# Optimization experiments

Measured on AMD Instinct MI355X. Metric: run time of the kernel, lower is better.

Reference implementation:

```python
import jax, jax.numpy as jnp
import numpy as np

N_NEAR = 16
BN_EPS = 1e-5


def fps(xyz, n_center):
    # farthest point sampling, deterministic start at index 0. xyz: [B,N,C]
    B, N, _ = xyz.shape
    dist0 = jnp.full((B, N), jnp.inf, dtype=xyz.dtype)
    far0 = jnp.zeros((B,), dtype=jnp.int32)

    def step(carry, _):
        dist, far = carry
        centroid = jnp.take_along_axis(xyz, far[:, None, None], axis=1)  # [B,1,C]
        d = jnp.sum((xyz - centroid) ** 2, axis=-1)                       # [B,N]
        dist = jnp.minimum(dist, d)
        nxt = jnp.argmax(dist, axis=-1).astype(jnp.int32)
        return (dist, nxt), far

    _, idxs = jax.lax.scan(step, (dist0, far0), None, length=n_center)
    return jnp.transpose(idxs)  # [B, n_center]


def knn(xyz, k):
    # k nearest neighbors (self included), xyz: [B,N,C] -> idx [B,N,k]
    sq = jnp.sum(xyz * xyz, axis=-1)
    d = sq[:, :, None] - 2.0 * jnp.einsum('bnc,bmc->bnm', xyz, xyz) + sq[:, None, :]
    _, idx = jax.lax.top_k(-d, k)
    return idx


def gather_points(x, idx):
    # x: [B,N,...], idx: [B,*dims] int -> [B,*dims,...]
    return jax.vmap(lambda xb, ib: xb[ib])(x, idx)


def conv_bn_relu(x, W, b, g, be):
    # x: [B,C,K,S]; 1x1 Conv2d + BatchNorm2d (training/batch stats) + ReLU
    y = jnp.einsum('oc,bcks->boks', W, x) + b[None, :, None, None]
    mean = jnp.mean(y, axis=(0, 2, 3), keepdims=True)
    var = jnp.mean((y - mean) ** 2, axis=(0, 2, 3), keepdims=True)  # biased var, as torch BN
    y = (y - mean) * jax.lax.rsqrt(var + BN_EPS)
    y = y * g[None, :, None, None] + be[None, :, None, None]
    return jax.nn.relu(y)


def setup_inputs() -> dict:
    key = jax.random.key(0)
    ks = jax.random.split(key, 8)
    B, N, EMB = 16, 2048, 64
    mlp = [64, 128, 256]
    in_ch = 2 + EMB
    inp = {
        'xy': jax.random.normal(ks[0], (B, 2, N), dtype=jnp.float32),
        'fea': jax.random.normal(ks[1], (B, EMB, N), dtype=jnp.float32),
    }
    last = in_ch
    for i, out in enumerate(mlp):
        inp[f'W{i+1}'] = 0.1 * jax.random.normal(ks[2 + i], (out, last), dtype=jnp.float32)
        inp[f'b{i+1}'] = jnp.zeros((out,), dtype=jnp.float32)
        inp[f'g{i+1}'] = jnp.ones((out,), dtype=jnp.float32)
        inp[f'be{i+1}'] = jnp.zeros((out,), dtype=jnp.float32)
        last = out
    return inp


def reference(xy, fea, W1, b1, g1, be1, W2, b2, g2, be2, W3, b3, g3, be3):
    B, _, N = xy.shape
    n_center = N // 2 + 1
    xyz = jnp.transpose(xy, (0, 2, 1))   # [B,N,2]
    f = jnp.transpose(fea, (0, 2, 1))    # [B,N,emb]

    fps_idx = fps(xyz, n_center)                      # [B,S]
    new_xyz = gather_points(xyz, fps_idx)             # [B,S,2]
    knn_idx = knn(xyz, N_NEAR)                        # [B,N,k]
    knn_of_fps = gather_points(knn_idx, fps_idx)      # [B,S,k]
    grouped_xyz = gather_points(xyz, knn_of_fps)      # [B,S,k,2]
    grouped_norm = grouped_xyz - new_xyz[:, :, None, :]
    grouped_f = gather_points(f, knn_of_fps)          # [B,S,k,emb]
    new_fea = jnp.concatenate([grouped_norm, grouped_f], axis=-1)  # [B,S,k,C]

    x = jnp.transpose(new_fea, (0, 3, 2, 1))          # [B,C,k,S]
    for (W, b, g, be) in ((W1, b1, g1, be1), (W2, b2, g2, be2), (W3, b3, g3, be3)):
        x = conv_bn_relu(x, W, b, g, be)
    out = jnp.max(x, axis=2)                          # [B,C_out,S]
    return jnp.transpose(new_xyz, (0, 2, 1)), out
```

## Files before the change

### kernel.cpp

```cpp
#include <hip/hip_runtime.h>
#include <math.h>

#define B_   16
#define N_   2048
#define S_   1025
#define K_   16
#define EMB_ 64
#define NF_  (B_ * S_ * K_)
#define NCH_ (NF_ / 64)
#define NBS_ (NCH_ * 4)

typedef float v2f __attribute__((ext_vector_type(2)));
typedef short bf16x8 __attribute__((ext_vector_type(8)));
typedef float f32x4 __attribute__((ext_vector_type(4)));

__device__ __forceinline__ unsigned short f2bf(float f) {
  unsigned u = __float_as_uint(f);
  u += 0x7fffu + ((u >> 16) & 1u);
  return (unsigned short)(u >> 16);
}
__device__ __forceinline__ float bfl(unsigned pk) { return __uint_as_float((pk & 0xffffu) << 16); }
__device__ __forceinline__ float bfh(unsigned pk) { return __uint_as_float(pk & 0xffff0000u); }

__global__ __launch_bounds__(256) __attribute__((amdgpu_waves_per_eu(1, 1)))
void fps_pk_kernel(const float* __restrict__ xy, const float* __restrict__ fea,
                   const float* __restrict__ W1,
                   const float* __restrict__ W2, const float* __restrict__ W3,
                   int* __restrict__ fps_idx, float* __restrict__ new_xyz,
                   float* __restrict__ out0, unsigned* __restrict__ Pp,
                   unsigned short* __restrict__ W2b, unsigned short* __restrict__ W3b) {
  __shared__ float smem[8192];
  if (blockIdx.x < 16) {
    const int b = blockIdx.x;
    float2* lxy = reinterpret_cast<float2*>(smem);
    const int lane = threadIdx.x;
    const float* xb = xy + (size_t)b * 2 * N_;
    v2f pxp[16], pyp[16];
    float dist[32];
    if (lane < 64) {
      const float2* xb2 = (const float2*)xb;
      const float2* yb2 = (const float2*)(xb + N_);
#pragma unroll
      for (int q = 0; q < 16; ++q) {
        float2 x01 = xb2[lane * 16 + q];
        float2 y01 = yb2[lane * 16 + q];
        int p = lane * 32 + 2 * q;
        lxy[p] = make_float2(x01.x, y01.x);
        lxy[p + 1] = make_float2(x01.y, y01.y);
        pxp[q][0] = x01.x; pxp[q][1] = x01.y;
        pyp[q][0] = y01.x; pyp[q][1] = y01.y;
        dist[2 * q] = __builtin_inff();
        dist[2 * q + 1] = __builtin_inff();
      }
#pragma unroll
      for (int q = 0; q < 16; ++q) {
        asm volatile("" : "+v"(pxp[q]), "+v"(pyp[q]));
      }
    }
    __syncthreads();
    if (lane < 64) {
      int cur = 0;
      for (int t = 0; t < S_; ++t) {
        float2 c = lxy[cur];
        if (lane == 0) {
          fps_idx[b * S_ + t] = cur;
          new_xyz[(b * S_ + t) * 2 + 0] = c.x;
          new_xyz[(b * S_ + t) * 2 + 1] = c.y;
          out0[b * 2 * S_ + t] = c.x;
          out0[b * 2 * S_ + S_ + t] = c.y;
        }
        const float ncx = -c.x, ncy = -c.y;
        v2f ncx2; ncx2[0] = ncx; ncx2[1] = ncx;
        v2f ncy2; ncy2[0] = ncy; ncy2[1] = ncy;
#pragma unroll
        for (int q = 0; q < 16; ++q) {
          v2f dx, dy, sx, sy, dd;
          asm("v_pk_add_f32 %0, %1, %2" : "=v"(dx) : "v"(pxp[q]), "v"(ncx2));
          asm("v_pk_add_f32 %0, %1, %2" : "=v"(dy) : "v"(pyp[q]), "v"(ncy2));
          asm("v_pk_mul_f32 %0, %1, %1" : "=v"(sx) : "v"(dx));
          asm("v_pk_mul_f32 %0, %1, %1" : "=v"(sy) : "v"(dy));
          asm("v_pk_add_f32 %0, %1, %2" : "=v"(dd) : "v"(sx), "v"(sy));
          dist[2 * q] = fminf(dist[2 * q], dd[0]);
          dist[2 * q + 1] = fminf(dist[2 * q + 1], dd[1]);
        }
        float m1[16], m2[8], m3[4], m4[2];
#pragma unroll
        for (int j = 0; j < 16; ++j) m1[j] = fmaxf(dist[2 * j], dist[2 * j + 1]);
#pragma unroll
        for (int j = 0; j < 8; ++j) m2[j] = fmaxf(m1[2 * j], m1[2 * j + 1]);
#pragma unroll
        for (int j = 0; j < 4; ++j) m3[j] = fmaxf(m2[2 * j], m2[2 * j + 1]);
        m4[0] = fmaxf(m3[0], m3[1]);
        m4[1] = fmaxf(m3[2], m3[3]);
        const float lmax = fmaxf(m4[0], m4[1]);
        int xr = __float_as_int(lmax);
#define DPP_MAX_STEP(CTRL)                                                        \
        {                                                                         \
          int tmp_ = __builtin_amdgcn_update_dpp(xr, xr, (CTRL), 0xF, 0xF, false);\
          xr = __float_as_int(fmaxf(__int_as_float(xr), __int_as_float(tmp_)));   \
        }
        DPP_MAX_STEP(0x111)
        DPP_MAX_STEP(0x112)
        DPP_MAX_STEP(0x114)
        DPP_MAX_STEP(0x118)
        DPP_MAX_STEP(0x142)
        DPP_MAX_STEP(0x143)
#undef DPP_MAX_STEP
        const float g = __int_as_float(__builtin_amdgcn_readlane(xr, 63));
        int n = (m4[0] == g) ? 0 : 1;
        float c3 = (n & 1) ? m3[2] : m3[0];
        n = 2 * n + ((c3 == g) ? 0 : 1);
        float lo2 = (n & 1) ? m2[2] : m2[0];
        float hi2 = (n & 1) ? m2[6] : m2[4];
        float c2 = (n & 2) ? hi2 : lo2;
        n = 2 * n + ((c2 == g) ? 0 : 1);
        float a0 = (n & 1) ? m1[2] : m1[0];
        float a1 = (n & 1) ? m1[6] : m1[4];
        float a2 = (n & 1) ? m1[10] : m1[8];
        float a3 = (n & 1) ? m1[14] : m1[12];
        float b0 = (n & 2) ? a1 : a0;
        float b1 = (n & 2) ? a3 : a2;
        float c1 = (n & 4) ? b1 : b0;
        n = 2 * n + ((c1 == g) ? 0 : 1);
        float e0 = (n & 1) ? dist[2] : dist[0];
        float e1 = (n & 1) ? dist[6] : dist[4];
        float e2 = (n & 1) ? dist[10] : dist[8];
        float e3 = (n & 1) ? dist[14] : dist[12];
        float e4 = (n & 1) ? dist[18] : dist[16];
        float e5 = (n & 1) ? dist[22] : dist[20];
        float e6 = (n & 1) ? dist[26] : dist[24];
        float e7 = (n & 1) ? dist[30] : dist[28];
        float f0 = (n & 2) ? e1 : e0;
        float f1 = (n & 2) ? e3 : e2;
        float f2 = (n & 2) ? e5 : e4;
        float f3 = (n & 2) ? e7 : e6;
        float g0 = (n & 4) ? f1 : f0;
        float g1 = (n & 4) ? f3 : f2;
        float c0 = (n & 8) ? g1 : g0;
        const int lf = 2 * n + ((c0 == g) ? 0 : 1);
        unsigned long long mask = __ballot(lmax == g);
        int first = __ffsll(mask) - 1;
        cur = __builtin_amdgcn_readlane(lane * 32 + lf, first);
      }
    }
  } else if (blockIdx.x < 528) {
    const int bid = blockIdx.x - 16;
    const int t = threadIdx.x;
    const int b = bid >> 5;
    const int pt0 = (bid & 31) << 6;
    float* W1L = smem;
    float* feaL = smem + 4096;
#pragma unroll
    for (int p = 0; p < 16; ++p) {
      int idx = t + 256 * p;
      int c = idx >> 6, e = idx & 63;
      W1L[e * 64 + c] = W1[c * 66 + 2 + e];
      int r = (t >> 6) + 4 * p, cc = t & 63;
      feaL[r * 64 + cc] = fea[((size_t)b * 64 + r) * N_ + pt0 + cc];
    }
    __syncthreads();
    const int tpt = t & 15, tcq = t >> 4;
    float acc[4][4];
#pragma unroll
    for (int i = 0; i < 4; ++i)
#pragma unroll
      for (int j = 0; j < 4; ++j) acc[i][j] = 0.f;
    for (int e = 0; e < 64; ++e) {
      float4 a4 = *reinterpret_cast<const float4*>(&W1L[e * 64 + tcq * 4]);
      float4 b4 = *reinterpret_cast<const float4*>(&feaL[e * 64 + tpt * 4]);
      const float av[4] = {a4.x, a4.y, a4.z, a4.w};
      const float bvv[4] = {b4.x, b4.y, b4.z, b4.w};
#pragma unroll
      for (int i = 0; i < 4; ++i)
#pragma unroll
        for (int j = 0; j < 4; ++j) acc[i][j] = fmaf(av[i], bvv[j], acc[i][j]);
    }
#pragma unroll
    for (int j = 0; j < 4; ++j) {
      int pt = tpt * 4 + j;
      unsigned lo = (unsigned)f2bf(acc[0][j]) | ((unsigned)f2bf(acc[1][j]) << 16);
      unsigned hi = (unsigned)f2bf(acc[2][j]) | ((unsigned)f2bf(acc[3][j]) << 16);
      unsigned* dst = &Pp[((size_t)(b * N_ + pt0 + pt)) * 32 + tcq * 2];
      dst[0] = lo;
      dst[1] = hi;
    }
  } else {
    const int t = threadIdx.x;
    for (int i = t; i < 128 * 64; i += 256) W2b[i] = f2bf(W2[i]);
    for (int i = t; i < 256 * 128; i += 256) W3b[i] = f2bf(W3[i]);
  }
}

__global__ __launch_bounds__(256) void knn_kernel(const float* __restrict__ xy,
                                                  const int* __restrict__ fps_idx,
                                                  int* __restrict__ knn_sel) {
  const int b = blockIdx.y;
  __shared__ float2 lxy[N_];
  __shared__ double lsq[N_];
  const float* xb = xy + (size_t)b * 2 * N_;
  for (int p = threadIdx.x; p < N_; p += 256) {
    float x = xb[p], y = xb[N_ + p];
    lxy[p] = make_float2(x, y);
    lsq[p] = (double)x * (double)x + (double)y * (double)y;
  }
  __syncthreads();
  const int t = threadIdx.x;
  const int s = blockIdx.x * 8 + (t >> 5);
  if (s >= S_) return;
  const int oct = t & 31;
  const int p0 = fps_idx[b * S_ + s];
  float2 q = lxy[p0];
  const double xn = (double)q.x, yn = (double)q.y;
  const double sqn = lsq[p0];
  double d16[16];
  int i16[16];
#pragma unroll
  for (int j = 0; j < 16; ++j) { d16[j] = __builtin_inf(); i16[j] = 0x7fffffff; }
  const int mlo = oct * 64;
  for (int m0 = mlo; m0 < mlo + 64; m0 += 4) {
    double dd[4];
#pragma unroll
    for (int u = 0; u < 4; ++u) {
      float2 p = lxy[m0 + u];
      double dot = (double)p.x * xn + (double)p.y * yn;
      dd[u] = (sqn - 2.0 * dot) + lsq[m0 + u];
    }
#pragma unroll
    for (int u = 0; u < 4; ++u) {
      if (dd[u] < d16[15]) {
        double d = dd[u];
        int mi = m0 + u;
#pragma unroll
        for (int j = 15; j >= 1; --j) {
          bool shift = d < d16[j - 1];
          bool ins = d < d16[j];
          d16[j] = shift ? d16[j - 1] : (ins ? d : d16[j]);
          i16[j] = shift ? i16[j - 1] : (ins ? mi : i16[j]);
        }
        if (d < d16[0]) { d16[0] = d; i16[0] = mi; }
      }
    }
  }
#pragma unroll
  for (int w = 1; w <= 16; w <<= 1) {
    double nd[16]; int ni[16];
#pragma unroll
    for (int i = 0; i < 16; ++i) {
      double rd = __shfl_xor(d16[15 - i], w, 64);
      int ri = __shfl_xor(i16[15 - i], w, 64);
      bool takeR = (rd < d16[i]) || (rd == d16[i] && ri < i16[i]);
      nd[i] = takeR ? rd : d16[i];
      ni[i] = takeR ? ri : i16[i];
    }
#pragma unroll
    for (int i = 0; i < 16; ++i) { d16[i] = nd[i]; i16[i] = ni[i]; }
    if (w < 16) {
#pragma unroll
      for (int dstg = 8; dstg >= 1; dstg >>= 1) {
#pragma unroll
        for (int i = 0; i < 16; ++i) {
          if ((i & dstg) == 0) {
            int a = i, c = i + dstg;
            bool sw = (d16[a] > d16[c]) || (d16[a] == d16[c] && i16[a] > i16[c]);
            double tlo = sw ? d16[c] : d16[a];
            double thi = sw ? d16[a] : d16[c];
            int ulo = sw ? i16[c] : i16[a];
            int uhi = sw ? i16[a] : i16[c];
            d16[a] = tlo; d16[c] = thi; i16[a] = ulo; i16[c] = uhi;
          }
        }
      }
    }
  }
  if (oct == 0) {
    int* dst = knn_sel + ((size_t)b * S_ + s) * K_;
#pragma unroll
    for (int j = 0; j < 16; ++j) dst[j] = i16[j];
  }
}

__global__ __launch_bounds__(256) void yk1_kernel(const float* __restrict__ xy,
                                                  const int* __restrict__ knn_sel,
                                                  const float* __restrict__ new_xyz,
                                                  const unsigned* __restrict__ Pp,
                                                  const float* __restrict__ W1,
                                                  const float* __restrict__ b1,
                                                  unsigned* __restrict__ Y1p) {
  __shared__ float w0s[64], w1s[64], bbs[64];
  const int t = threadIdx.x;
  if (t < 64) { w0s[t] = W1[t * 66 + 0]; w1s[t] = W1[t * 66 + 1]; bbs[t] = b1[t]; }
  __syncthreads();
  const int n = blockIdx.x * 256 + t;
  const int bs = n >> 4;
  const int b = bs / S_;
  const int nbr = knn_sel[n];
  const float dx = xy[(size_t)b * 2 * N_ + nbr] - new_xyz[bs * 2 + 0];
  const float dy = xy[(size_t)b * 2 * N_ + N_ + nbr] - new_xyz[bs * 2 + 1];
  const unsigned* prow = &Pp[((size_t)(b * N_ + nbr)) * 32];
#pragma unroll 8
  for (int j = 0; j < 32; ++j) {
    unsigned pj = prow[j];
    int c = 2 * j;
    float v0 = bfl(pj) + w0s[c] * dx + w1s[c] * dy + bbs[c];
    float v1 = bfh(pj) + w0s[c + 1] * dx + w1s[c + 1] * dy + bbs[c + 1];
    Y1p[(size_t)j * NF_ + n] = (unsigned)f2bf(v0) | ((unsigned)f2bf(v1) << 16);
  }
}

__global__ __launch_bounds__(256) void rowstats_kernel(const unsigned* __restrict__ Y1p,
                                                       float* __restrict__ parts) {
  const int j = blockIdx.x & 31;
  const int seg = blockIdx.x >> 5;
  const int SEG = NF_ / 8;
  const unsigned* p = Y1p + (size_t)j * NF_ + (size_t)seg * SEG;
  double s0 = 0, q0 = 0, s1 = 0, q1 = 0;
  for (int i = threadIdx.x; i < SEG; i += 256) {
    unsigned pk = p[i];
    double a = (double)bfl(pk), b = (double)bfh(pk);
    s0 += a; q0 = fma(a, a, q0);
    s1 += b; q1 = fma(b, b, q1);
  }
  __shared__ double sh[4][256];
  sh[0][threadIdx.x] = s0; sh[1][threadIdx.x] = q0;
  sh[2][threadIdx.x] = s1; sh[3][threadIdx.x] = q1;
  __syncthreads();
  for (int o = 128; o > 0; o >>= 1) {
    if (threadIdx.x < o) {
#pragma unroll
      for (int u = 0; u < 4; ++u) sh[u][threadIdx.x] += sh[u][threadIdx.x + o];
    }
    __syncthreads();
  }
  if (threadIdx.x == 0) {
    float* dst = parts + (size_t)(j * 8 + seg) * 4;
    dst[0] = (float)sh[0][0];
    dst[1] = (float)sh[2][0];
    dst[2] = (float)sh[1][0];
    dst[3] = (float)sh[3][0];
  }
}

__global__ void redabsch1_kernel(const float* __restrict__ parts,
                                 const float* __restrict__ g, const float* __restrict__ be,
                                 float* __restrict__ A, float* __restrict__ D) {
  int m = threadIdx.x;
  if (m >= 64) return;
  int j = m >> 1, par = m & 1;
  double a = 0.0, b = 0.0;
  for (int seg = 0; seg < 8; ++seg) {
    const float* src = parts + (size_t)(j * 8 + seg) * 4;
    a += (double)src[par];
    b += (double)src[2 + par];
  }
  double mu = a * (1.0 / NF_);
  double var = b * (1.0 / NF_) - mu * mu;
  double aa = (double)g[m] / sqrt(var + 1e-5);
  A[m] = (float)aa;
  D[m] = (float)((double)be[m] - aa * mu);
}

__global__ void redabsch_kernel(const float* __restrict__ parts, int P, int M,
                                const float* __restrict__ g, const float* __restrict__ be,
                                float* __restrict__ A, float* __restrict__ D) {
  int m = threadIdx.x;
  if (m >= M) return;
  double a = 0.0, b = 0.0;
  for (int p = 0; p < P; ++p) {
    a += (double)parts[(size_t)p * 2 * M + m];
    b += (double)parts[(size_t)p * 2 * M + M + m];
  }
  double mu = a * (1.0 / NF_);
  double var = b * (1.0 / NF_) - mu * mu;
  double aa = (double)g[m] / sqrt(var + 1e-5);
  A[m] = (float)aa;
  D[m] = (float)((double)be[m] - aa * mu);
}

__device__ __forceinline__ float rowsum16(float v) {
#define RADD(CTRL) { int tm_ = __builtin_amdgcn_update_dpp(0, __float_as_int(v), (CTRL), 0xF, 0xF, true); \
                     v += __int_as_float(tm_); }
  RADD(0x111) RADD(0x112) RADD(0x114) RADD(0x118)
#undef RADD
  return v;
}

__device__ __forceinline__ void stage_x1(const unsigned* Y1p, const float* ab1, char* x1c,
                                         size_t n0, int w, int L) {
#pragma unroll
  for (int e = 0; e < 8; ++e) {
    int k0 = 2 * (w + 4 * e);
    unsigned pkv = Y1p[(size_t)(k0 >> 1) * NF_ + n0 + L];
    float v0 = fmaxf(fmaf(bfl(pkv), ab1[k0], ab1[64 + k0]), 0.f);
    float v1 = fmaxf(fmaf(bfh(pkv), ab1[k0 + 1], ab1[64 + k0 + 1]), 0.f);
    unsigned pk = (unsigned)f2bf(v0) | ((unsigned)f2bf(v1) << 16);
    *reinterpret_cast<unsigned*>(&x1c[L * 128 + ((2 * k0) ^ ((L & 7) << 4))]) = pk;
  }
}

__global__ __launch_bounds__(256) void passA_mfma_kernel(
    const unsigned* __restrict__ Y1p, const unsigned short* __restrict__ W2b,
    const float* __restrict__ A1v, const float* __restrict__ Bc1v,
    float* __restrict__ parts) {
  __shared__ float ab1[128];
  __shared__ __align__(16) unsigned short x1b[64 * 64];
  const int t = threadIdx.x;
  const int w = t >> 6, L = t & 63;
  if (t < 128) ab1[t] = (t < 64) ? A1v[t] : Bc1v[t - 64];
  bf16x8 w2f[2][2];
#pragma unroll
  for (int rb = 0; rb < 2; ++rb)
#pragma unroll
    for (int ks = 0; ks < 2; ++ks) {
      int row = (2 * w + rb) * 16 + (L & 15);
      int koff = ks * 32 + (L >> 4) * 8;
      w2f[rb][ks] = *reinterpret_cast<const bf16x8*>(&W2b[row * 64 + koff]);
    }
  float vs[2][4], vq[2][4];
#pragma unroll
  for (int rb = 0; rb < 2; ++rb)
#pragma unroll
    for (int r = 0; r < 4; ++r) { vs[rb][r] = 0.f; vq[rb][r] = 0.f; }
  char* x1c = reinterpret_cast<char*>(x1b);
  for (int ch = blockIdx.x; ch < NCH_; ch += 512) {
    const size_t n0 = (size_t)ch * 64;
    __syncthreads();
    stage_x1(Y1p, ab1, x1c, n0, w, L);
    __syncthreads();
#pragma unroll
    for (int rb = 0; rb < 2; ++rb) {
      f32x4 acc2[4];
#pragma unroll
      for (int cb = 0; cb < 4; ++cb) acc2[cb][0] = acc2[cb][1] = acc2[cb][2] = acc2[cb][3] = 0.f;
#pragma unroll
      for (int ks = 0; ks < 2; ++ks)
#pragma unroll
        for (int cb = 0; cb < 4; ++cb) {
          int n = cb * 16 + (L & 15);
          int koff = ks * 32 + (L >> 4) * 8;
          bf16x8 bfr = *reinterpret_cast<const bf16x8*>(&x1c[n * 128 + ((2 * koff) ^ ((n & 7) << 4))]);
          acc2[cb] = __builtin_amdgcn_mfma_f32_16x16x32_bf16(w2f[rb][ks], bfr, acc2[cb], 0, 0, 0);
        }
#pragma unroll
      for (int cb = 0; cb < 4; ++cb)
#pragma unroll
        for (int r = 0; r < 4; ++r) {
          float y = acc2[cb][r];
          vs[rb][r] += y;
          vq[rb][r] = fmaf(y, y, vq[rb][r]);
        }
    }
  }
#pragma unroll
  for (int rb = 0; rb < 2; ++rb)
#pragma unroll
    for (int r = 0; r < 4; ++r) {
      float s = rowsum16(vs[rb][r]);
      float q = rowsum16(vq[rb][r]);
      if ((L & 15) == 15) {
        int row = (2 * w + rb) * 16 + (L >> 4) * 4 + r;
        parts[(size_t)blockIdx.x * 256 + row] = s;
        parts[(size_t)blockIdx.x * 256 + 128 + row] = q;
      }
    }
}

__global__ __launch_bounds__(256) void passB_mfma_kernel(
    const unsigned* __restrict__ Y1p,
    const unsigned short* __restrict__ W2b, const unsigned short* __restrict__ W3b,
    const float* __restrict__ A1v, const float* __restrict__ Bc1v,
    const float* __restrict__ A2v, const float* __restrict__ D2v,
    float* __restrict__ parts, unsigned* __restrict__ M3) {
  __shared__ float ab1[128];
  __shared__ __align__(16) unsigned short x1b[64 * 64];
  __shared__ __align__(16) unsigned short x2b[64 * 128];
  const int t = threadIdx.x;
  const int w = t >> 6, L = t & 63;
  if (t < 128) ab1[t] = (t < 64) ? A1v[t] : Bc1v[t - 64];
  bf16x8 w3f[4][4];
#pragma unroll
  for (int rb = 0; rb < 4; ++rb)
#pragma unroll
    for (int ks = 0; ks < 4; ++ks) {
      int row = (4 * w + rb) * 16 + (L & 15);
      int koff = ks * 32 + (L >> 4) * 8;
      w3f[rb][ks] = *reinterpret_cast<const bf16x8*>(&W3b[row * 128 + koff]);
    }
  bf16x8 w2f[2][2];
#pragma unroll
  for (int rb = 0; rb < 2; ++rb)
#pragma unroll
    for (int ks = 0; ks < 2; ++ks) {
      int row = (2 * w + rb) * 16 + (L & 15);
      int koff = ks * 32 + (L >> 4) * 8;
      w2f[rb][ks] = *reinterpret_cast<const bf16x8*>(&W2b[row * 64 + koff]);
    }
  float vs[4][4], vq[4][4];
#pragma unroll
  for (int rb = 0; rb < 4; ++rb)
#pragma unroll
    for (int r = 0; r < 4; ++r) { vs[rb][r] = 0.f; vq[rb][r] = 0.f; }
  char* x1c = reinterpret_cast<char*>(x1b);
  char* x2c = reinterpret_cast<char*>(x2b);
  for (int ch = blockIdx.x; ch < NCH_; ch += 256) {
    const size_t n0 = (size_t)ch * 64;
    __syncthreads();
    stage_x1(Y1p, ab1, x1c, n0, w, L);
    __syncthreads();
#pragma unroll
    for (int rb = 0; rb < 2; ++rb) {
      f32x4 acc2[4];
#pragma unroll
      for (int cb = 0; cb < 4; ++cb) acc2[cb][0] = acc2[cb][1] = acc2[cb][2] = acc2[cb][3] = 0.f;
#pragma unroll
      for (int ks = 0; ks < 2; ++ks)
#pragma unroll
        for (int cb = 0; cb < 4; ++cb) {
          int n = cb * 16 + (L & 15);
          int koff = ks * 32 + (L >> 4) * 8;
          bf16x8 bfr = *reinterpret_cast<const bf16x8*>(&x1c[n * 128 + ((2 * koff) ^ ((n & 7) << 4))]);
          acc2[cb] = __builtin_amdgcn_mfma_f32_16x16x32_bf16(w2f[rb][ks], bfr, acc2[cb], 0, 0, 0);
        }
#pragma unroll
      for (int cb = 0; cb < 4; ++cb) {
        int n = cb * 16 + (L & 15);
        int kbase = (2 * w + rb) * 16 + (L >> 4) * 4;
#pragma unroll
        for (int rp = 0; rp < 2; ++rp) {
          int r0 = 2 * rp;
          float a0 = A2v[kbase + r0], d0 = D2v[kbase + r0];
          float a1 = A2v[kbase + r0 + 1], d1 = D2v[kbase + r0 + 1];
          float v0 = fmaxf(fmaf(acc2[cb][r0], a0, d0), 0.f);
          float v1 = fmaxf(fmaf(acc2[cb][r0 + 1], a1, d1), 0.f);
          unsigned pk = (unsigned)f2bf(v0) | ((unsigned)f2bf(v1) << 16);
          int k0 = kbase + r0;
          *reinterpret_cast<unsigned*>(&x2c[n * 256 + ((2 * k0) ^ ((n & 7) << 4))]) = pk;
        }
      }
    }
    __syncthreads();
    bf16x8 b3[4][4];
#pragma unroll
    for (int cb = 0; cb < 4; ++cb)
#pragma unroll
      for (int ks = 0; ks < 4; ++ks) {
        int n = cb * 16 + (L & 15);
        int koff = ks * 32 + (L >> 4) * 8;
        b3[cb][ks] = *reinterpret_cast<const bf16x8*>(&x2c[n * 256 + ((2 * koff) ^ ((n & 7) << 4))]);
      }
#pragma unroll
    for (int rb = 0; rb < 4; ++rb) {
      f32x4 acc3[4];
#pragma unroll
      for (int cb = 0; cb < 4; ++cb) acc3[cb][0] = acc3[cb][1] = acc3[cb][2] = acc3[cb][3] = 0.f;
#pragma unroll
      for (int ks = 0; ks < 4; ++ks)
#pragma unroll
        for (int cb = 0; cb < 4; ++cb)
          acc3[cb] = __builtin_amdgcn_mfma_f32_16x16x32_bf16(w3f[rb][ks], b3[cb][ks], acc3[cb], 0, 0, 0);
#pragma unroll
      for (int cb = 0; cb < 4; ++cb)
#pragma unroll
        for (int r = 0; r < 4; ++r) {
          float y = acc3[cb][r];
          vs[rb][r] += y;
          vq[rb][r] = fmaf(y, y, vq[rb][r]);
        }
      {
        int rowbase = (4 * w + rb) * 16 + (L >> 4) * 4;
#pragma unroll
        for (int cb = 0; cb < 4; ++cb) {
#pragma unroll
          for (int r = 0; r < 4; ++r) {
            float v = acc3[cb][r];
            int xi = __float_as_int(v), xm = __float_as_int(v);
#define RMAX(CTRL) { int tm_ = __builtin_amdgcn_update_dpp(xi, xi, (CTRL), 0xF, 0xF, false); \
                     xi = __float_as_int(fmaxf(__int_as_float(xi), __int_as_float(tm_))); }
#define RMIN(CTRL) { int tm_ = __builtin_amdgcn_update_dpp(xm, xm, (CTRL), 0xF, 0xF, false); \
                     xm = __float_as_int(fminf(__int_as_float(xm), __int_as_float(tm_))); }
            RMAX(0x111) RMAX(0x112) RMAX(0x114) RMAX(0x118)
            RMIN(0x111) RMIN(0x112) RMIN(0x114) RMIN(0x118)
#undef RMAX
#undef RMIN
            if ((L & 15) == 15) {
              int row = rowbase + r;
              int bs = ch * 4 + cb;
              M3[(size_t)row * NBS_ + bs] =
                  (unsigned)f2bf(__int_as_float(xi)) | ((unsigned)f2bf(__int_as_float(xm)) << 16);
            }
          }
        }
      }
    }
  }
#pragma unroll
  for (int rb = 0; rb < 4; ++rb)
#pragma unroll
    for (int r = 0; r < 4; ++r) {
      float s = rowsum16(vs[rb][r]);
      float q = rowsum16(vq[rb][r]);
      if ((L & 15) == 15) {
        int row = (4 * w + rb) * 16 + (L >> 4) * 4 + r;
        parts[(size_t)blockIdx.x * 512 + row] = s;
        parts[(size_t)blockIdx.x * 512 + 256 + row] = q;
      }
    }
}

__global__ __launch_bounds__(256) void final_small_kernel(
    const unsigned* __restrict__ M3, const float* __restrict__ A3,
    const float* __restrict__ D3, float* __restrict__ out1) {
  int gid = blockIdx.x * 256 + threadIdx.x;
  int row = gid / NBS_, bs = gid - row * NBS_;
  unsigned pk = M3[gid];
  float vmax = bfl(pk);
  float vmin = bfh(pk);
  float a = A3[row];
  float v = (a >= 0.f) ? vmax : vmin;
  int b = bs / S_, s = bs - b * S_;
  out1[((size_t)(b * 256 + row)) * S_ + s] = fmaxf(fmaf(v, a, D3[row]), 0.f);
}

__global__ void diag_kernel(float* out, float v) {
  if (threadIdx.x == 0 && blockIdx.x == 0) out[0] = v;
}

extern "C" void kernel_launch(void* const* d_in, const int* in_sizes, int n_in,
                              void* d_out, int out_size, void* d_ws, size_t ws_size,
                              hipStream_t stream) {
  const float* xy  = (const float*)d_in[0];
  const float* fea = (const float*)d_in[1];
  const float* W1  = (const float*)d_in[2];
  const float* b1  = (const float*)d_in[3];
  const float* g1  = (const float*)d_in[4];
  const float* be1 = (const float*)d_in[5];
  const float* W2  = (const float*)d_in[6];
  const float* g2  = (const float*)d_in[8];
  const float* be2 = (const float*)d_in[9];
  const float* W3  = (const float*)d_in[10];
  const float* g3  = (const float*)d_in[12];
  const float* be3 = (const float*)d_in[13];
  float* out = (float*)d_out;
  float* out1 = out + B_ * 2 * S_;

  char* w = (char*)d_ws;
  size_t off = 0;
  auto take = [&](size_t bytes) -> void* {
    void* p = w + off;
    off += (bytes + 255) & ~(size_t)255;
    return p;
  };
  int*      fps_idx = (int*)take((size_t)B_ * S_ * 4);
  float*    new_xyz = (float*)take((size_t)B_ * S_ * 2 * 4);
  int*      knn_sel = (int*)take((size_t)NF_ * 4);
  unsigned* Pp      = (unsigned*)take((size_t)B_ * N_ * 32 * 4);
  unsigned* Y1p     = (unsigned*)take((size_t)32 * NF_ * 4);
  float*    parts1  = (float*)take((size_t)256 * 4 * 4);
  float*    A1      = (float*)take(64 * 4);
  float*    Bc1     = (float*)take(64 * 4);
  float*    partsA  = (float*)take((size_t)512 * 256 * 4);
  float*    A2      = (float*)take(128 * 4);
  float*    D2      = (float*)take(128 * 4);
  float*    partsB  = (float*)take((size_t)256 * 512 * 4);
  float*    A3      = (float*)take(256 * 4);
  float*    D3      = (float*)take(256 * 4);
  unsigned short* W2b = (unsigned short*)take((size_t)128 * 64 * 2);
  unsigned short* W3b = (unsigned short*)take((size_t)256 * 128 * 2);
  unsigned* M3      = (unsigned*)take((size_t)256 * NBS_ * 4);

  if (off > ws_size) {
    diag_kernel<<<1, 64, 0, stream>>>(out, (float)(ws_size >> 20));
    return;
  }

  fps_pk_kernel<<<16 + 512 + 1, 256, 0, stream>>>(xy, fea, W1, W2, W3,
                                                  fps_idx, new_xyz, out, Pp, W2b, W3b);
  knn_kernel<<<dim3((S_ + 7) / 8, B_), 256, 0, stream>>>(xy, fps_idx, knn_sel);
  yk1_kernel<<<NF_ / 256, 256, 0, stream>>>(xy, knn_sel, new_xyz, Pp, W1, b1, Y1p);

  rowstats_kernel<<<256, 256, 0, stream>>>(Y1p, parts1);
  redabsch1_kernel<<<1, 64, 0, stream>>>(parts1, g1, be1, A1, Bc1);

  passA_mfma_kernel<<<512, 256, 0, stream>>>(Y1p, W2b, A1, Bc1, partsA);
  redabsch_kernel<<<1, 128, 0, stream>>>(partsA, 512, 128, g2, be2, A2, D2);

  passB_mfma_kernel<<<256, 256, 0, stream>>>(Y1p, W2b, W3b, A1, Bc1, A2, D2, partsB, M3);
  redabsch_kernel<<<1, 256, 0, stream>>>(partsB, 256, 256, g3, be3, A3, D3);

  final_small_kernel<<<(256 * NBS_) / 256, 256, 0, stream>>>(M3, A3, D3, out1);
}
```

Before: 1.351 ms.

## Fuse FPS, projection and kNN into a persistent kernel with progress flags

Merges the FPS/projection kernel and the kNN kernel into one persistent kernel of 256 blocks. Sixteen blocks run FPS and publish progress counters every 32 centers. The remaining blocks pull work items from atomic counters: first the W1·fea projection and bf16 weight conversion, then kNN tiles that spin-wait until FPS has produced the centers they need. This is meant to overlap kNN with the long serial FPS loop instead of running kNN afterwards. In exchange it adds a memset, atomics and busy-waiting, and it relies on all FPS blocks being co-resident so the waiting blocks cannot deadlock.

```diff
diff --git a/kernel.cpp b/kernel.cpp
--- a/kernel.cpp
+++ b/kernel.cpp
@@ -9,10 +9,18 @@
 #define NF_  (B_ * S_ * K_)
 #define NCH_ (NF_ / 64)
 #define NBS_ (NCH_ * 4)
+#define NBLK 256
+#define PK_UNITS 513
+#define KNN_ITEMS (129 * 16)
 
 typedef float v2f __attribute__((ext_vector_type(2)));
 typedef short bf16x8 __attribute__((ext_vector_type(8)));
 typedef float f32x4 __attribute__((ext_vector_type(4)));
+
+#define AL(p)    __hip_atomic_load((p), __ATOMIC_ACQUIRE, __HIP_MEMORY_SCOPE_AGENT)
+#define ALR(p)   __hip_atomic_load((p), __ATOMIC_RELAXED, __HIP_MEMORY_SCOPE_AGENT)
+#define ASR(p,v) __hip_atomic_store((p), (v), __ATOMIC_RELEASE, __HIP_MEMORY_SCOPE_AGENT)
+#define AADD(p)  __hip_atomic_fetch_add((p), 1, __ATOMIC_ACQ_REL, __HIP_MEMORY_SCOPE_AGENT)
 
 __device__ __forceinline__ unsigned short f2bf(float f) {
   unsigned u = __float_as_uint(f);
@@ -22,18 +30,37 @@
 __device__ __forceinline__ float bfl(unsigned pk) { return __uint_as_float((pk & 0xffffu) << 16); }
 __device__ __forceinline__ float bfh(unsigned pk) { return __uint_as_float(pk & 0xffff0000u); }
 
-__global__ __launch_bounds__(256) __attribute__((amdgpu_waves_per_eu(1, 1)))
-void fps_pk_kernel(const float* __restrict__ xy, const float* __restrict__ fea,
+__device__ __forceinline__ float rowsum16(float v) {
+#define RADD(CTRL) { int tm_ = __builtin_amdgcn_update_dpp(0, __float_as_int(v), (CTRL), 0xF, 0xF, true); \
+                     v += __int_as_float(tm_); }
+  RADD(0x111) RADD(0x112) RADD(0x114) RADD(0x118)
+#undef RADD
+  return v;
+}
+
+__global__ void diag_kernel(float* out, float v) {
+  if (threadIdx.x == 0 && blockIdx.x == 0) out[0] = v;
+}
+
+__global__ __launch_bounds__(256, 1)
+void phase0_kernel(const float* __restrict__ xy, const float* __restrict__ fea,
                    const float* __restrict__ W1,
                    const float* __restrict__ W2, const float* __restrict__ W3,
-                   int* __restrict__ fps_idx, float* __restrict__ new_xyz,
-                   float* __restrict__ out0, unsigned* __restrict__ Pp,
-                   unsigned short* __restrict__ W2b, unsigned short* __restrict__ W3b) {
-  __shared__ float smem[8192];
-  if (blockIdx.x < 16) {
-    const int b = blockIdx.x;
-    float2* lxy = reinterpret_cast<float2*>(smem);
-    const int lane = threadIdx.x;
+                   int* fps_idx, float* new_xyz, int* knn_sel,
+                   unsigned* Pp, unsigned short* W2b, unsigned short* W3b,
+                   float* out0, int* flags) {
+  __shared__ float2 sh_lxy[N_];
+  __shared__ double sh_lsq[N_];
+  __shared__ float sh_pkA[4096];
+  __shared__ float sh_pkB[4096];
+  __shared__ int sh_unit;
+  const int bid = blockIdx.x;
+  const int tid = threadIdx.x;
+  int* progress = flags + 8;
+
+  if (bid < 16) {
+    const int b = bid;
+    const int lane = tid;
     const float* xb = xy + (size_t)b * 2 * N_;
     v2f pxp[16], pyp[16];
     float dist[32];
@@ -45,8 +72,8 @@
         float2 x01 = xb2[lane * 16 + q];
         float2 y01 = yb2[lane * 16 + q];
         int p = lane * 32 + 2 * q;
-        lxy[p] = make_float2(x01.x, y01.x);
-        lxy[p + 1] = make_float2(x01.y, y01.y);
+        sh_lxy[p] = make_float2(x01.x, y01.x);
+        sh_lxy[p + 1] = make_float2(x01.y, y01.y);
         pxp[q][0] = x01.x; pxp[q][1] = x01.y;
         pyp[q][0] = y01.x; pyp[q][1] = y01.y;
         dist[2 * q] = __builtin_inff();
@@ -61,7 +88,7 @@
     if (lane < 64) {
       int cur = 0;
       for (int t = 0; t < S_; ++t) {
-        float2 c = lxy[cur];
+        float2 c = sh_lxy[cur];
         if (lane == 0) {
           fps_idx[b * S_ + t] = cur;
           new_xyz[(b * S_ + t) * 2 + 0] = c.x;
@@ -115,12 +142,12 @@
         float c2 = (n & 2) ? hi2 : lo2;
         n = 2 * n + ((c2 == g) ? 0 : 1);
         float a0 = (n & 1) ? m1[2] : m1[0];
-        float a1 = (n & 1) ? m1[6] : m1[4];
-        float a2 = (n & 1) ? m1[10] : m1[8];
-        float a3 = (n & 1) ? m1[14] : m1[12];
-        float b0 = (n & 2) ? a1 : a0;
-        float b1 = (n & 2) ? a3 : a2;
-        float c1 = (n & 4) ? b1 : b0;
+        float a1v = (n & 1) ? m1[6] : m1[4];
+        float a2v = (n & 1) ? m1[10] : m1[8];
+        float a3v = (n & 1) ? m1[14] : m1[12];
+        float b0 = (n & 2) ? a1v : a0;
+        float b1v = (n & 2) ? a3v : a2v;
+        float c1 = (n & 4) ? b1v : b0;
         n = 2 * n + ((c1 == g) ? 0 : 1);
         float e0 = (n & 1) ? dist[2] : dist[0];
         float e1 = (n & 1) ? dist[6] : dist[4];
@@ -135,147 +162,160 @@
         float f2 = (n & 2) ? e5 : e4;
         float f3 = (n & 2) ? e7 : e6;
         float g0 = (n & 4) ? f1 : f0;
-        float g1 = (n & 4) ? f3 : f2;
-        float c0 = (n & 8) ? g1 : g0;
+        float g1v = (n & 4) ? f3 : f2;
+        float c0 = (n & 8) ? g1v : g0;
         const int lf = 2 * n + ((c0 == g) ? 0 : 1);
         unsigned long long mask = __ballot(lmax == g);
         int first = __ffsll(mask) - 1;
         cur = __builtin_amdgcn_readlane(lane * 32 + lf, first);
-      }
-    }
-  } else if (blockIdx.x < 528) {
-    const int bid = blockIdx.x - 16;
-    const int t = threadIdx.x;
-    const int b = bid >> 5;
-    const int pt0 = (bid & 31) << 6;
-    float* W1L = smem;
-    float* feaL = smem + 4096;
-#pragma unroll
-    for (int p = 0; p < 16; ++p) {
-      int idx = t + 256 * p;
-      int c = idx >> 6, e = idx & 63;
-      W1L[e * 64 + c] = W1[c * 66 + 2 + e];
-      int r = (t >> 6) + 4 * p, cc = t & 63;
-      feaL[r * 64 + cc] = fea[((size_t)b * 64 + r) * N_ + pt0 + cc];
-    }
-    __syncthreads();
-    const int tpt = t & 15, tcq = t >> 4;
-    float acc[4][4];
-#pragma unroll
-    for (int i = 0; i < 4; ++i)
-#pragma unroll
-      for (int j = 0; j < 4; ++j) acc[i][j] = 0.f;
-    for (int e = 0; e < 64; ++e) {
-      float4 a4 = *reinterpret_cast<const float4*>(&W1L[e * 64 + tcq * 4]);
-      float4 b4 = *reinterpret_cast<const float4*>(&feaL[e * 64 + tpt * 4]);
-      const float av[4] = {a4.x, a4.y, a4.z, a4.w};
-      const float bvv[4] = {b4.x, b4.y, b4.z, b4.w};
-#pragma unroll
-      for (int i = 0; i < 4; ++i)
-#pragma unroll
-        for (int j = 0; j < 4; ++j) acc[i][j] = fmaf(av[i], bvv[j], acc[i][j]);
-    }
-#pragma unroll
-    for (int j = 0; j < 4; ++j) {
-      int pt = tpt * 4 + j;
-      unsigned lo = (unsigned)f2bf(acc[0][j]) | ((unsigned)f2bf(acc[1][j]) << 16);
-      unsigned hi = (unsigned)f2bf(acc[2][j]) | ((unsigned)f2bf(acc[3][j]) << 16);
-      unsigned* dst = &Pp[((size_t)(b * N_ + pt0 + pt)) * 32 + tcq * 2];
-      dst[0] = lo;
-      dst[1] = hi;
+        if (lane == 0 && ((t & 31) == 31 || t == S_ - 1)) {
+          ASR(&progress[b], t + 1);
+        }
+      }
     }
   } else {
-    const int t = threadIdx.x;
-    for (int i = t; i < 128 * 64; i += 256) W2b[i] = f2bf(W2[i]);
-    for (int i = t; i < 256 * 128; i += 256) W3b[i] = f2bf(W3[i]);
-  }
-}
-
-__global__ __launch_bounds__(256) void knn_kernel(const float* __restrict__ xy,
-                                                  const int* __restrict__ fps_idx,
-                                                  int* __restrict__ knn_sel) {
-  const int b = blockIdx.y;
-  __shared__ float2 lxy[N_];
-  __shared__ double lsq[N_];
-  const float* xb = xy + (size_t)b * 2 * N_;
-  for (int p = threadIdx.x; p < N_; p += 256) {
-    float x = xb[p], y = xb[N_ + p];
-    lxy[p] = make_float2(x, y);
-    lsq[p] = (double)x * (double)x + (double)y * (double)y;
-  }
-  __syncthreads();
-  const int t = threadIdx.x;
-  const int s = blockIdx.x * 8 + (t >> 5);
-  if (s >= S_) return;
-  const int oct = t & 31;
-  const int p0 = fps_idx[b * S_ + s];
-  float2 q = lxy[p0];
-  const double xn = (double)q.x, yn = (double)q.y;
-  const double sqn = lsq[p0];
-  double d16[16];
-  int i16[16];
-#pragma unroll
-  for (int j = 0; j < 16; ++j) { d16[j] = __builtin_inf(); i16[j] = 0x7fffffff; }
-  const int mlo = oct * 64;
-  for (int m0 = mlo; m0 < mlo + 64; m0 += 4) {
-    double dd[4];
-#pragma unroll
-    for (int u = 0; u < 4; ++u) {
-      float2 p = lxy[m0 + u];
-      double dot = (double)p.x * xn + (double)p.y * yn;
-      dd[u] = (sqn - 2.0 * dot) + lsq[m0 + u];
-    }
-#pragma unroll
-    for (int u = 0; u < 4; ++u) {
-      if (dd[u] < d16[15]) {
-        double d = dd[u];
-        int mi = m0 + u;
-#pragma unroll
-        for (int j = 15; j >= 1; --j) {
-          bool shift = d < d16[j - 1];
-          bool ins = d < d16[j];
-          d16[j] = shift ? d16[j - 1] : (ins ? d : d16[j]);
-          i16[j] = shift ? i16[j - 1] : (ins ? mi : i16[j]);
-        }
-        if (d < d16[0]) { d16[0] = d; i16[0] = mi; }
-      }
-    }
-  }
-#pragma unroll
-  for (int w = 1; w <= 16; w <<= 1) {
-    double nd[16]; int ni[16];
-#pragma unroll
-    for (int i = 0; i < 16; ++i) {
-      double rd = __shfl_xor(d16[15 - i], w, 64);
-      int ri = __shfl_xor(i16[15 - i], w, 64);
-      bool takeR = (rd < d16[i]) || (rd == d16[i] && ri < i16[i]);
-      nd[i] = takeR ? rd : d16[i];
-      ni[i] = takeR ? ri : i16[i];
-    }
-#pragma unroll
-    for (int i = 0; i < 16; ++i) { d16[i] = nd[i]; i16[i] = ni[i]; }
-    if (w < 16) {
-#pragma unroll
-      for (int dstg = 8; dstg >= 1; dstg >>= 1) {
-#pragma unroll
-        for (int i = 0; i < 16; ++i) {
-          if ((i & dstg) == 0) {
-            int a = i, c = i + dstg;
-            bool sw = (d16[a] > d16[c]) || (d16[a] == d16[c] && i16[a] > i16[c]);
-            double tlo = sw ? d16[c] : d16[a];
-            double thi = sw ? d16[a] : d16[c];
-            int ulo = sw ? i16[c] : i16[a];
-            int uhi = sw ? i16[a] : i16[c];
-            d16[a] = tlo; d16[c] = thi; i16[a] = ulo; i16[c] = uhi;
+    for (;;) {
+      __syncthreads();
+      if (tid == 0) sh_unit = AADD(&flags[2]);
+      __syncthreads();
+      int u = sh_unit;
+      if (u >= PK_UNITS) break;
+      if (u < 512) {
+        const int b = u >> 5;
+        const int pt0 = (u & 31) << 6;
+#pragma unroll
+        for (int p = 0; p < 16; ++p) {
+          int idx = tid + 256 * p;
+          int c = idx >> 6, e = idx & 63;
+          sh_pkA[e * 64 + c] = W1[c * 66 + 2 + e];
+          int r = (tid >> 6) + 4 * p, cc = tid & 63;
+          sh_pkB[r * 64 + cc] = fea[((size_t)b * 64 + r) * N_ + pt0 + cc];
+        }
+        __syncthreads();
+        const int tpt = tid & 15, tcq = tid >> 4;
+        float acc[4][4];
+#pragma unroll
+        for (int i = 0; i < 4; ++i)
+#pragma unroll
+          for (int j = 0; j < 4; ++j) acc[i][j] = 0.f;
+        for (int e = 0; e < 64; ++e) {
+          float4 a4 = *reinterpret_cast<const float4*>(&sh_pkA[e * 64 + tcq * 4]);
+          float4 b4 = *reinterpret_cast<const float4*>(&sh_pkB[e * 64 + tpt * 4]);
+          const float av[4] = {a4.x, a4.y, a4.z, a4.w};
+          const float bvv[4] = {b4.x, b4.y, b4.z, b4.w};
+#pragma unroll
+          for (int i = 0; i < 4; ++i)
+#pragma unroll
+            for (int j = 0; j < 4; ++j) acc[i][j] = fmaf(av[i], bvv[j], acc[i][j]);
+        }
+#pragma unroll
+        for (int j = 0; j < 4; ++j) {
+          int pt = tpt * 4 + j;
+          unsigned lo = (unsigned)f2bf(acc[0][j]) | ((unsigned)f2bf(acc[1][j]) << 16);
+          unsigned hi = (unsigned)f2bf(acc[2][j]) | ((unsigned)f2bf(acc[3][j]) << 16);
+          unsigned* dst = &Pp[((size_t)(b * N_ + pt0 + pt)) * 32 + tcq * 2];
+          dst[0] = lo;
+          dst[1] = hi;
+        }
+      } else {
+        for (int i = tid; i < 128 * 64; i += 256) W2b[i] = f2bf(W2[i]);
+        for (int i = tid; i < 256 * 128; i += 256) W3b[i] = f2bf(W3[i]);
+      }
+    }
+    for (;;) {
+      __syncthreads();
+      if (tid == 0) sh_unit = AADD(&flags[4]);
+      __syncthreads();
+      int it = sh_unit;
+      if (it >= KNN_ITEMS) break;
+      const int b = it & 15;
+      const int s0 = (it >> 4) * 8;
+      const int sHi = (s0 + 8 < S_) ? (s0 + 8) : S_;
+      if (tid == 0) {
+        while (AL(&progress[b]) < sHi) __builtin_amdgcn_s_sleep(8);
+      }
+      __syncthreads();
+      const float* xb = xy + (size_t)b * 2 * N_;
+      for (int p = tid; p < N_; p += 256) {
+        float x = xb[p], y = xb[N_ + p];
+        sh_lxy[p] = make_float2(x, y);
+        sh_lsq[p] = (double)x * (double)x + (double)y * (double)y;
+      }
+      __syncthreads();
+      const int s = s0 + (tid >> 5);
+      const int oct = tid & 31;
+      if (s < S_) {
+        const int p0 = ALR((int*)&fps_idx[b * S_ + s]);
+        float2 q = sh_lxy[p0];
+        const double xn = (double)q.x, yn = (double)q.y;
+        const double sqn = sh_lsq[p0];
+        double d16[16];
+        int i16[16];
+#pragma unroll
+        for (int j = 0; j < 16; ++j) { d16[j] = __builtin_inf(); i16[j] = 0x7fffffff; }
+        const int mlo = oct * 64;
+        for (int m0 = mlo; m0 < mlo + 64; m0 += 4) {
+          double dd[4];
+#pragma unroll
+          for (int u2 = 0; u2 < 4; ++u2) {
+            float2 p = sh_lxy[m0 + u2];
+            double dot = (double)p.x * xn + (double)p.y * yn;
+            dd[u2] = (sqn - 2.0 * dot) + sh_lsq[m0 + u2];
           }
-        }
-      }
-    }
-  }
-  if (oct == 0) {
-    int* dst = knn_sel + ((size_t)b * S_ + s) * K_;
-#pragma unroll
-    for (int j = 0; j < 16; ++j) dst[j] = i16[j];
+#pragma unroll
+          for (int u2 = 0; u2 < 4; ++u2) {
+            if (dd[u2] < d16[15]) {
+              double d = dd[u2];
+              int mi = m0 + u2;
+#pragma unroll
+              for (int j = 15; j >= 1; --j) {
+                bool shift = d < d16[j - 1];
+                bool ins = d < d16[j];
+                d16[j] = shift ? d16[j - 1] : (ins ? d : d16[j]);
+                i16[j] = shift ? i16[j - 1] : (ins ? mi : i16[j]);
+              }
+              if (d < d16[0]) { d16[0] = d; i16[0] = mi; }
+            }
+          }
+        }
+#pragma unroll
+        for (int w = 1; w <= 16; w <<= 1) {
+          double nd[16]; int ni[16];
+#pragma unroll
+          for (int i = 0; i < 16; ++i) {
+            double rd = __shfl_xor(d16[15 - i], w, 64);
+            int ri = __shfl_xor(i16[15 - i], w, 64);
+            bool takeR = (rd < d16[i]) || (rd == d16[i] && ri < i16[i]);
+            nd[i] = takeR ? rd : d16[i];
+            ni[i] = takeR ? ri : i16[i];
+          }
+#pragma unroll
+          for (int i = 0; i < 16; ++i) { d16[i] = nd[i]; i16[i] = ni[i]; }
+          if (w < 16) {
+#pragma unroll
+            for (int dstg = 8; dstg >= 1; dstg >>= 1) {
+#pragma unroll
+              for (int i = 0; i < 16; ++i) {
+                if ((i & dstg) == 0) {
+                  int a = i, c = i + dstg;
+                  bool sw = (d16[a] > d16[c]) || (d16[a] == d16[c] && i16[a] > i16[c]);
+                  double tlo = sw ? d16[c] : d16[a];
+                  double thi = sw ? d16[a] : d16[c];
+                  int ulo = sw ? i16[c] : i16[a];
+                  int uhi = sw ? i16[a] : i16[c];
+                  d16[a] = tlo; d16[c] = thi; i16[a] = ulo; i16[c] = uhi;
+                }
+              }
+            }
+          }
+        }
+        if (oct == 0) {
+          int* dst = knn_sel + ((size_t)b * S_ + s) * K_;
+#pragma unroll
+          for (int j = 0; j < 16; ++j) dst[j] = i16[j];
+        }
+      }
+    }
   }
 }
 
@@ -376,14 +416,6 @@
   D[m] = (float)((double)be[m] - aa * mu);
 }
 
-__device__ __forceinline__ float rowsum16(float v) {
-#define RADD(CTRL) { int tm_ = __builtin_amdgcn_update_dpp(0, __float_as_int(v), (CTRL), 0xF, 0xF, true); \
-                     v += __int_as_float(tm_); }
-  RADD(0x111) RADD(0x112) RADD(0x114) RADD(0x118)
-#undef RADD
-  return v;
-}
-
 __device__ __forceinline__ void stage_x1(const unsigned* Y1p, const float* ab1, char* x1c,
                                          size_t n0, int w, int L) {
 #pragma unroll
@@ -620,10 +652,6 @@
   out1[((size_t)(b * 256 + row)) * S_ + s] = fmaxf(fmaf(v, a, D3[row]), 0.f);
 }
 
-__global__ void diag_kernel(float* out, float v) {
-  if (threadIdx.x == 0 && blockIdx.x == 0) out[0] = v;
-}
-
 extern "C" void kernel_launch(void* const* d_in, const int* in_sizes, int n_in,
                               void* d_out, int out_size, void* d_ws, size_t ws_size,
                               hipStream_t stream) {
@@ -649,6 +677,7 @@
     off += (bytes + 255) & ~(size_t)255;
     return p;
   };
+  int*      flags   = (int*)take(256);
   int*      fps_idx = (int*)take((size_t)B_ * S_ * 4);
   float*    new_xyz = (float*)take((size_t)B_ * S_ * 2 * 4);
   int*      knn_sel = (int*)take((size_t)NF_ * 4);
@@ -672,9 +701,9 @@
     return;
   }
 
-  fps_pk_kernel<<<16 + 512 + 1, 256, 0, stream>>>(xy, fea, W1, W2, W3,
-                                                  fps_idx, new_xyz, out, Pp, W2b, W3b);
-  knn_kernel<<<dim3((S_ + 7) / 8, B_), 256, 0, stream>>>(xy, fps_idx, knn_sel);
+  hipMemsetAsync(flags, 0, 256, stream);
+  phase0_kernel<<<NBLK, 256, 0, stream>>>(xy, fea, W1, W2, W3, fps_idx, new_xyz,
+                                          knn_sel, Pp, W2b, W3b, out, flags);
   yk1_kernel<<<NF_ / 256, 256, 0, stream>>>(xy, knn_sel, new_xyz, Pp, W1, b1, Y1p);
 
   rowstats_kernel<<<256, 256, 0, stream>>>(Y1p, parts1);
```

Measured after the change: 1.234 ms. -8.7%, faster.
